# Optimization experiments

Measured on AMD Instinct MI355X. Metric: run time of the kernel, lower is better.

## Reference

```python
import jax, jax.numpy as jnp
import numpy as np

N_NODES = 10000
N_EDGES = 320000
D = 128
H = 4
C = 128
L = 2
NEG_SLOPE = 0.2
LN_EPS = 1e-5


def setup_inputs() -> dict:
    key = jax.random.key(0)
    ks = jax.random.split(key, 8)
    x = jax.random.normal(ks[0], (N_NODES, D), dtype=jnp.float32)
    edge_index = jax.random.randint(ks[1], (2, N_EDGES), 0, N_NODES, dtype=jnp.int64)
    # weights scaled ~Glorot to keep attention logits in a sane range
    Wl = jax.random.normal(ks[2], (L, D, H * C), dtype=jnp.float32) * 0.1
    Wr = jax.random.normal(ks[3], (L, D, H * C), dtype=jnp.float32) * 0.1
    att = jax.random.normal(ks[4], (L, H, C), dtype=jnp.float32) * 0.1
    return {
        "x": x,
        "edge_index": edge_index,
        "Wl": Wl,
        "bl": jnp.zeros((L, H * C), jnp.float32),
        "Wr": Wr,
        "br": jnp.zeros((L, H * C), jnp.float32),
        "att": att,
        "bias": jnp.zeros((L, D), jnp.float32),
        "ln_g": jnp.ones((L, D), jnp.float32),
        "ln_b": jnp.zeros((L, D), jnp.float32),
    }


def _gatv2_layer(x, src, dst, Wl, bl, Wr, br, att, b):
    """GATv2Conv (concat=False -> head mean), messages src->dst, softmax over dst."""
    n = x.shape[0]
    xl = (x @ Wl + bl).reshape(n, H, C)  # source transform
    xr = (x @ Wr + br).reshape(n, H, C)  # target transform
    s = jax.nn.leaky_relu(xl[src] + xr[dst], NEG_SLOPE)  # [E, H, C]
    e = jnp.einsum("ehc,hc->eh", s, att)  # attention logits [E, H]
    m = jax.ops.segment_max(e, dst, num_segments=n)  # stable softmax per dst segment
    ex = jnp.exp(e - m[dst])
    denom = jax.ops.segment_sum(ex, dst, num_segments=n)
    alpha = ex / denom[dst]  # [E, H]
    out = jax.ops.segment_sum(alpha[:, :, None] * xl[src], dst, num_segments=n)  # [N, H, C]
    return out.mean(axis=1) + b  # concat=False -> mean over heads, then bias


def _layer_norm(h, g, b):
    mu = h.mean(-1, keepdims=True)
    var = ((h - mu) ** 2).mean(-1, keepdims=True)
    return (h - mu) * jax.lax.rsqrt(var + LN_EPS) * g + b


def reference(x, edge_index, Wl, bl, Wr, br, att, bias, ln_g, ln_b):
    n = x.shape[0]
    loop = jnp.arange(n, dtype=edge_index.dtype)
    src = jnp.concatenate([edge_index[0], loop])  # add self-loops (PyG default)
    dst = jnp.concatenate([edge_index[1], loop])
    for i in range(L):
        h = _gatv2_layer(x, src, dst, Wl[i], bl[i], Wr[i], br[i], att[i], bias[i])
        x = h + x  # residual
        x = jax.nn.relu(_layer_norm(x, ln_g[i], ln_b[i]))
    return x
```

## Files before the change

### kernel.cpp

```cpp
#include <hip/hip_runtime.h>
#include <math.h>

#define N_NODES 10000
#define N_EDGES 320000
#define E_TOT   (N_EDGES + N_NODES)
#define NEG 0.2f
#define CAP 96

typedef short bf16x8 __attribute__((ext_vector_type(8)));
typedef float f32x4 __attribute__((ext_vector_type(4)));
typedef float f32x2 __attribute__((ext_vector_type(2)));

static __device__ __forceinline__ float4 ld4g(const float* p) { return *(const float4*)p; }

static __device__ __forceinline__ uint4 ldg4(const unsigned short* p, unsigned byteoff) {
    return *(const uint4*)((const char*)p + byteoff);
}
static __device__ __forceinline__ int ldgi(const int* p, int e) { return p[e]; }

static __device__ __forceinline__ unsigned short f2b(float f) {
    unsigned u;
    __builtin_memcpy(&u, &f, 4);
    unsigned r = (u + 0x7fffu + ((u >> 16) & 1u)) >> 16;
    return (unsigned short)r;
}
static __device__ __forceinline__ f32x2 unpk(unsigned d) {
    f32x2 r;
    r.x = __uint_as_float(d << 16);
    r.y = __uint_as_float(d & 0xffff0000u);
    return r;
}

template <int CTRL>
static __device__ __forceinline__ float dpp_add_step(float x) {
    int y = __builtin_amdgcn_update_dpp(0, __float_as_int(x), CTRL, 0xf, 0xf, true);
    return x + __int_as_float(y);
}
static __device__ __forceinline__ float row_sum16(float x) {
    x = dpp_add_step<0x121>(x);
    x = dpp_add_step<0x122>(x);
    x = dpp_add_step<0x124>(x);
    x = dpp_add_step<0x128>(x);
    return x;
}

static __device__ __forceinline__ void comp_full(
    uint4 u,
    const f32x2* __restrict__ xr2, const f32x2* __restrict__ at2,
    f32x2* __restrict__ acc2, float* __restrict__ dsum) {
    const f32x2 neg2 = {NEG, NEG};
    const unsigned* w = (const unsigned*)&u;
    f32x2 F[4];
#pragma unroll
    for (int q = 0; q < 4; ++q) F[q] = unpk(w[q]);
    f32x2 qq = {0.f, 0.f};
#pragma unroll
    for (int q = 0; q < 4; ++q) {
        f32x2 s = F[q] + xr2[q];
        s = __builtin_elementwise_max(s, s * neg2);
        qq = __builtin_elementwise_fma(s, at2[q], qq);
    }
    float ev = __expf(row_sum16(qq.x + qq.y));
    *dsum += ev;
    f32x2 W = {ev, ev};
#pragma unroll
    for (int q = 0; q < 4; ++q)
        acc2[q] = __builtin_elementwise_fma(F[q], W, acc2[q]);
}

static __device__ __forceinline__ void comp_mask(
    uint4 u, bool valid,
    const f32x2* __restrict__ xr2, const f32x2* __restrict__ at2,
    f32x2* __restrict__ acc2, float* __restrict__ dsum) {
    const f32x2 neg2 = {NEG, NEG};
    const unsigned* w = (const unsigned*)&u;
    f32x2 F[4];
#pragma unroll
    for (int q = 0; q < 4; ++q) F[q] = unpk(w[q]);
    f32x2 qq = {0.f, 0.f};
#pragma unroll
    for (int q = 0; q < 4; ++q) {
        f32x2 s = F[q] + xr2[q];
        s = __builtin_elementwise_max(s, s * neg2);
        qq = __builtin_elementwise_fma(s, at2[q], qq);
    }
    float ev = __expf(row_sum16(qq.x + qq.y));
    ev = valid ? ev : 0.f;
    *dsum += ev;
    f32x2 W = {ev, ev};
#pragma unroll
    for (int q = 0; q < 4; ++q)
        acc2[q] = __builtin_elementwise_fma(F[q], W, acc2[q]);
}

__global__ __launch_bounds__(256) void prep_fused_kernel(
    const float* __restrict__ x,
    const float* __restrict__ Wl, const float* __restrict__ Wr,
    unsigned short* __restrict__ xb, unsigned short* __restrict__ WT,
    int* __restrict__ deg) {
    int tid = threadIdx.x, bid = blockIdx.x;
    __shared__ float tbuf[32][33];

    for (int i = bid * 256 + tid; i < N_NODES; i += 256 * 256) deg[i] = 0;

    int l = bid >> 7;
    int rest = bid & 127;
    int ky = rest >> 5, nx = rest & 31;
    int n0 = nx * 32, k0 = ky * 32;
    const float* S = ((n0 < 512) ? Wl : Wr) + (size_t)l * 65536;
    int nn0 = n0 & 511;
    int tx = tid & 31, ty = tid >> 5;
#pragma unroll
    for (int it = 0; it < 4; ++it) {
        int k = k0 + ty + it * 8;
        tbuf[ty + it * 8][tx] = S[(size_t)k * 512 + nn0 + tx];
    }
    __syncthreads();
    unsigned short* dstp = WT + (size_t)l * 1024 * 128;
#pragma unroll
    for (int it = 0; it < 4; ++it) {
        int n = n0 + ty + it * 8;
        int k = k0 + tx;
        dstp[(size_t)n * 128 + k] = f2b(tbuf[tx][ty + it * 8]);
    }
    for (int i = bid * 256 + tid; i < N_NODES * 32; i += 256 * 256) {
        float4 v = ld4g(x + 4 * i);
        ushort4 o = make_ushort4(f2b(v.x), f2b(v.y), f2b(v.z), f2b(v.w));
        *(ushort4*)(xb + 4 * i) = o;
    }
}

template <int DO_FILL>
__global__ __launch_bounds__(256) void gemm_mfma_kernel(const unsigned short* __restrict__ A,
                                                        const unsigned short* __restrict__ Bt,
                                                        const float* __restrict__ bl,
                                                        const float* __restrict__ br,
                                                        unsigned short* __restrict__ xlh,
                                                        unsigned short* __restrict__ xrh,
                                                        const int* __restrict__ ei,
                                                        int* __restrict__ deg,
                                                        int* __restrict__ csr_src) {
    __shared__ unsigned short As[2][64][72];
    int tid = threadIdx.x;
    int wave = tid >> 6, lane = tid & 63;
    int l15 = lane & 15, quad = lane >> 4;
    int row0 = blockIdx.y * 64, col0 = blockIdx.x * 128;
    const float* bias = (col0 < 512) ? (bl + col0) : (br + col0 - 512);

#pragma unroll
    for (int it = 0; it < 4; ++it) {
        int e = tid + it * 256;
        int r = e >> 4, s = e & 15;
        int gr = row0 + r;
        bf16x8 v = (bf16x8)(short)0;
        if (gr < N_NODES) v = *(const bf16x8*)(A + (size_t)gr * 128 + s * 8);
        *(bf16x8*)&As[s >> 3][r][(s & 7) * 8] = v;
    }
    __syncthreads();

    f32x4 acc[8];
#pragma unroll
    for (int ni = 0; ni < 8; ++ni)
#pragma unroll
        for (int r = 0; r < 4; ++r) acc[ni][r] = 0.f;

    const unsigned short* Bbase = Bt + (size_t)col0 * 128;
    unsigned bvo = (unsigned)(l15 * 256 + quad * 16);

#pragma unroll
    for (int kc = 0; kc < 2; ++kc) {
#pragma unroll
        for (int kq = 0; kq < 2; ++kq) {
            bf16x8 af = *(const bf16x8*)&As[kc][wave * 16 + l15][kq * 32 + quad * 8];
            bf16x8 bfr[8];
#pragma unroll
            for (int ni = 0; ni < 8; ++ni) {
                uint4 u = ldg4(Bbase, bvo + (unsigned)(ni * 4096 + kc * 128 + kq * 64));
                __builtin_memcpy(&bfr[ni], &u, 16);
            }
#pragma unroll
            for (int ni = 0; ni < 8; ++ni)
                acc[ni] = __builtin_amdgcn_mfma_f32_16x16x32_bf16(af, bfr[ni], acc[ni], 0, 0, 0);
        }
    }

    float bv[8];
#pragma unroll
    for (int ni = 0; ni < 8; ++ni) bv[ni] = bias[ni * 16 + l15];

    int h = (col0 >> 7) & 3;
    unsigned short* dstb = ((col0 < 512) ? xlh : xrh) + (((size_t)h * N_NODES) << 7);

#pragma unroll
    for (int r = 0; r < 4; ++r) {
        int grow = row0 + wave * 16 + quad * 4 + r;
        if (grow >= N_NODES) continue;
#pragma unroll
        for (int ni = 0; ni < 8; ++ni)
            dstb[((size_t)grow << 7) + ni * 16 + l15] = f2b(acc[ni][r] + bv[ni]);
    }

    if (DO_FILL) {
        bool is64 = ((ei[1] | ei[3] | ei[5] | ei[7]) == 0);
        int nthreads = gridDim.x * gridDim.y * 256;
        int gid = (blockIdx.y * gridDim.x + blockIdx.x) * 256 + tid;
        for (int i = gid; i < E_TOT; i += nthreads) {
            int src, dst;
            if (i < N_EDGES) {
                if (is64) { const long long* e = (const long long*)ei; src = (int)e[i]; dst = (int)e[N_EDGES + i]; }
                else { src = ei[i]; dst = ei[N_EDGES + i]; }
            } else {
                src = dst = i - N_EDGES;
            }
            int pos = atomicAdd(&deg[dst], 1);
            if (pos < CAP) csr_src[dst * CAP + pos] = src;
        }
    }
}

__global__ __launch_bounds__(256) void attn_kernel(
    const unsigned short* __restrict__ xlh,
    const unsigned short* __restrict__ xrh,
    const int* __restrict__ deg, const int* __restrict__ csr_src,
    const float* __restrict__ att,
    float* __restrict__ hpart) {
    int tid = threadIdx.x;
    unsigned bid = blockIdx.x;
    int w = tid >> 6, lane = tid & 63;
    int head = __builtin_amdgcn_readfirstlane((int)((bid & 7u) >> 1));
    int slot = (int)((bid >> 3) * 2 + (bid & 1u));
    int e = lane >> 4, g = lane & 15;
    unsigned gboff = (unsigned)(g << 4);

    const unsigned short* XL = xlh + (((size_t)head * N_NODES) << 7);
    const unsigned short* XR = xrh + (((size_t)head * N_NODES) << 7);
    float* HP = hpart + (((size_t)head * N_NODES) << 7);

    f32x2 at2[4];
    {
        const float* ap = att + head * 128 + g * 8;
        float4 a = ld4g(ap);
        float4 b = ld4g(ap + 4);
        at2[0].x = a.x; at2[0].y = a.y; at2[1].x = a.z; at2[1].y = a.w;
        at2[2].x = b.x; at2[2].y = b.y; at2[3].x = b.z; at2[3].y = b.w;
    }

    for (int dst0 = slot * 4 + w; dst0 < N_NODES; dst0 += 2048) {
        int dst = __builtin_amdgcn_readfirstlane(dst0);

        f32x2 xr2[4];
        {
            uint4 u = *(const uint4*)(XR + ((size_t)dst << 7) + g * 8);
            xr2[0] = unpk(u.x); xr2[1] = unpk(u.y); xr2[2] = unpk(u.z); xr2[3] = unpk(u.w);
        }

        int len = deg[dst];
        if (len > CAP) len = CAP;
        const int* cp = csr_src + dst * CAP;
        int full = len >> 2, rem = len & 3;

        float d = 0.f;
        f32x2 acc2[4] = {{0.f, 0.f}, {0.f, 0.f}, {0.f, 0.f}, {0.f, 0.f}};

        if (full) {
            int idx = ldgi(cp, e);
            uint4 uc = ldg4(XL, ((unsigned)idx << 8) + gboff);
            for (int r = 0; r + 1 < full; ++r) {
                int i1 = ldgi(cp + 4 * (r + 1), e);
                uint4 un = ldg4(XL, ((unsigned)i1 << 8) + gboff);
                comp_full(uc, xr2, at2, acc2, &d);
                uc = un;
            }
            comp_full(uc, xr2, at2, acc2, &d);
        }
        if (rem) {
            int raw = ldgi(cp + 4 * full, e);
            int idx = (e < rem) ? raw : 0;
            uint4 u = ldg4(XL, ((unsigned)idx << 8) + gboff);
            comp_mask(u, e < rem, xr2, at2, acc2, &d);
        }

        float t[8];
#pragma unroll
        for (int q = 0; q < 4; ++q) { t[2 * q] = acc2[q].x; t[2 * q + 1] = acc2[q].y; }
#pragma unroll
        for (int j = 0; j < 8; ++j) {
            t[j] += __shfl_xor(t[j], 16, 64);
            t[j] += __shfl_xor(t[j], 32, 64);
        }
        float ds = d;
        ds += __shfl_xor(ds, 16, 64);
        ds += __shfl_xor(ds, 32, 64);
        float inv = 1.f / ds;
#pragma unroll
        for (int j = 0; j < 8; ++j) t[j] *= inv;

        if (lane < 16) {
            float* op = HP + ((size_t)dst << 7) + g * 8;
            *(float4*)op = make_float4(t[0], t[1], t[2], t[3]);
            *(float4*)(op + 4) = make_float4(t[4], t[5], t[6], t[7]);
        }
    }
}

__global__ __launch_bounds__(256) void combine_kernel(
    const float* __restrict__ hpart, const float* __restrict__ x_in,
    const float* __restrict__ bias, const float* __restrict__ ln_g,
    const float* __restrict__ ln_b, float* __restrict__ x_out,
    unsigned short* __restrict__ xb_out) {
    int wv = (blockIdx.x * blockDim.x + threadIdx.x) >> 6;
    if (wv >= N_NODES) return;
    int lane = threadIdx.x & 63;
    int dst = __builtin_amdgcn_readfirstlane(wv);
    int c = lane * 2;
    const float* hp = hpart + ((size_t)dst << 7) + c;
    const size_t hs = ((size_t)N_NODES) << 7;
    f32x2 h0 = *(const f32x2*)(hp);
    f32x2 h1 = *(const f32x2*)(hp + hs);
    f32x2 h2 = *(const f32x2*)(hp + 2 * hs);
    f32x2 h3 = *(const f32x2*)(hp + 3 * hs);
    f32x2 bi = *(const f32x2*)(bias + c);
    f32x2 xi = *(const f32x2*)(x_in + ((size_t)dst << 7) + c);
    f32x2 hc = ((h0 + h1) + (h2 + h3)) * 0.25f + bi + xi;
    float sm = hc.x + hc.y;
    float sq = hc.x * hc.x + hc.y * hc.y;
    sm = row_sum16(sm); sm += __shfl_xor(sm, 16, 64); sm += __shfl_xor(sm, 32, 64);
    sq = row_sum16(sq); sq += __shfl_xor(sq, 16, 64); sq += __shfl_xor(sq, 32, 64);
    float mu = sm * (1.f / 128.f);
    float var = sq * (1.f / 128.f) - mu * mu;
    float rs = rsqrtf(var + 1e-5f);
    f32x2 gg = *(const f32x2*)(ln_g + c);
    f32x2 bb = *(const f32x2*)(ln_b + c);
    float y0 = fmaxf((hc.x - mu) * rs * gg.x + bb.x, 0.f);
    float y1 = fmaxf((hc.y - mu) * rs * gg.y + bb.y, 0.f);
    f32x2 y = {y0, y1};
    *(f32x2*)(x_out + ((size_t)dst << 7) + c) = y;
    if (xb_out) {
        unsigned pk = ((unsigned)f2b(y0)) | (((unsigned)f2b(y1)) << 16);
        *(unsigned*)(xb_out + ((size_t)dst << 7) + c) = pk;
    }
}

extern "C" void kernel_launch(void* const* d_in, const int* in_sizes, int n_in,
                              void* d_out, int out_size, void* d_ws, size_t ws_size,
                              hipStream_t stream) {
    const float* x    = (const float*)d_in[0];
    const int*   ei   = (const int*)d_in[1];
    const float* Wl   = (const float*)d_in[2];
    const float* bl   = (const float*)d_in[3];
    const float* Wr   = (const float*)d_in[4];
    const float* br   = (const float*)d_in[5];
    const float* att  = (const float*)d_in[6];
    const float* bias = (const float*)d_in[7];
    const float* lng  = (const float*)d_in[8];
    const float* lnb  = (const float*)d_in[9];
    float* out = (float*)d_out;

    char* ws = (char*)d_ws;
    unsigned short* xlh = (unsigned short*)ws; ws += (size_t)4 * N_NODES * 128 * 2;
    unsigned short* xrh = (unsigned short*)ws; ws += (size_t)4 * N_NODES * 128 * 2;
    float* hpart = (float*)ws;          ws += (size_t)4 * N_NODES * 128 * 4;
    float* xbuf  = (float*)ws;          ws += (size_t)N_NODES * 128 * 4;
    unsigned short* xb = (unsigned short*)ws; ws += (size_t)N_NODES * 128 * 2;
    unsigned short* WT = (unsigned short*)ws; ws += (size_t)2 * 1024 * 128 * 2;
    int* deg     = (int*)ws;            ws += (size_t)N_NODES * 4;
    int* csr_src = (int*)ws;            ws += (size_t)N_NODES * CAP * 4;

    prep_fused_kernel<<<256, 256, 0, stream>>>(x, Wl, Wr, xb, WT, deg);

    for (int l = 0; l < 2; ++l) {
        const float* xin = (l == 0) ? x : xbuf;
        float* xout = (l == 0) ? xbuf : out;
        unsigned short* xbo = (l == 0) ? xb : (unsigned short*)nullptr;
        if (l == 0)
            gemm_mfma_kernel<1><<<dim3(8, 157), 256, 0, stream>>>(
                xb, WT, bl, br, xlh, xrh, ei, deg, csr_src);
        else
            gemm_mfma_kernel<0><<<dim3(8, 157), 256, 0, stream>>>(
                xb, WT + (size_t)1024 * 128, bl + 512, br + 512, xlh, xrh, ei, deg, csr_src);
        attn_kernel<<<2048, 256, 0, stream>>>(
            xlh, xrh, deg, csr_src, att + (size_t)l * 512, hpart);
        combine_kernel<<<2500, 256, 0, stream>>>(
            hpart, xin, bias + (size_t)l * 128,
            lng + (size_t)l * 128, lnb + (size_t)l * 128, xout, xbo);
    }
}
```

Before: 239.5 us.

## Stage weight tile in LDS and load A fragments directly in MFMA GEMM

```diff
diff --git a/kernel.cpp b/kernel.cpp
--- a/kernel.cpp
+++ b/kernel.cpp
@@ -140,47 +140,58 @@
                                                         const int* __restrict__ ei,
                                                         int* __restrict__ deg,
                                                         int* __restrict__ csr_src) {
-    __shared__ unsigned short As[2][64][72];
+    __shared__ unsigned short Bs[2][128][72];
     int tid = threadIdx.x;
     int wave = tid >> 6, lane = tid & 63;
     int l15 = lane & 15, quad = lane >> 4;
-    int row0 = blockIdx.y * 64, col0 = blockIdx.x * 128;
+    int row0 = blockIdx.y * 128, col0 = blockIdx.x * 128;
     const float* bias = (col0 < 512) ? (bl + col0) : (br + col0 - 512);
 
-#pragma unroll
-    for (int it = 0; it < 4; ++it) {
-        int e = tid + it * 256;
-        int r = e >> 4, s = e & 15;
-        int gr = row0 + r;
-        bf16x8 v = (bf16x8)(short)0;
-        if (gr < N_NODES) v = *(const bf16x8*)(A + (size_t)gr * 128 + s * 8);
-        *(bf16x8*)&As[s >> 3][r][(s & 7) * 8] = v;
-    }
+    bf16x8 st[8];
+    {
+        const unsigned short* src = Bt + (size_t)(col0 + (tid >> 1)) * 128 + (size_t)(tid & 1) * 64;
+#pragma unroll
+        for (int j = 0; j < 8; ++j) st[j] = *(const bf16x8*)(src + j * 8);
+    }
+
+    bf16x8 af[2][2][2];
+#pragma unroll
+    for (int mi = 0; mi < 2; ++mi) {
+        int row = row0 + wave * 32 + mi * 16 + l15;
+        int rr = (row < N_NODES) ? row : 0;
+        const unsigned short* ap = A + ((size_t)rr << 7);
+#pragma unroll
+        for (int kc = 0; kc < 2; ++kc)
+#pragma unroll
+            for (int kq = 0; kq < 2; ++kq)
+                af[mi][kc][kq] = *(const bf16x8*)(ap + kc * 64 + kq * 32 + quad * 8);
+    }
+
+#pragma unroll
+    for (int j = 0; j < 8; ++j) *(bf16x8*)&Bs[tid & 1][tid >> 1][j * 8] = st[j];
     __syncthreads();
 
-    f32x4 acc[8];
-#pragma unroll
-    for (int ni = 0; ni < 8; ++ni)
-#pragma unroll
-        for (int r = 0; r < 4; ++r) acc[ni][r] = 0.f;
-
-    const unsigned short* Bbase = Bt + (size_t)col0 * 128;
-    unsigned bvo = (unsigned)(l15 * 256 + quad * 16);
+    f32x4 acc[2][8];
+#pragma unroll
+    for (int mi = 0; mi < 2; ++mi)
+#pragma unroll
+        for (int ni = 0; ni < 8; ++ni)
+#pragma unroll
+            for (int r = 0; r < 4; ++r) acc[mi][ni][r] = 0.f;
 
 #pragma unroll
     for (int kc = 0; kc < 2; ++kc) {
 #pragma unroll
         for (int kq = 0; kq < 2; ++kq) {
-            bf16x8 af = *(const bf16x8*)&As[kc][wave * 16 + l15][kq * 32 + quad * 8];
             bf16x8 bfr[8];
 #pragma unroll
-            for (int ni = 0; ni < 8; ++ni) {
-                uint4 u = ldg4(Bbase, bvo + (unsigned)(ni * 4096 + kc * 128 + kq * 64));
-                __builtin_memcpy(&bfr[ni], &u, 16);
-            }
-#pragma unroll
             for (int ni = 0; ni < 8; ++ni)
-                acc[ni] = __builtin_amdgcn_mfma_f32_16x16x32_bf16(af, bfr[ni], acc[ni], 0, 0, 0);
+                bfr[ni] = *(const bf16x8*)&Bs[kc][ni * 16 + l15][kq * 32 + quad * 8];
+#pragma unroll
+            for (int mi = 0; mi < 2; ++mi)
+#pragma unroll
+                for (int ni = 0; ni < 8; ++ni)
+                    acc[mi][ni] = __builtin_amdgcn_mfma_f32_16x16x32_bf16(af[mi][kc][kq], bfr[ni], acc[mi][ni], 0, 0, 0);
         }
     }
 
@@ -192,12 +203,15 @@
     unsigned short* dstb = ((col0 < 512) ? xlh : xrh) + (((size_t)h * N_NODES) << 7);
 
 #pragma unroll
-    for (int r = 0; r < 4; ++r) {
-        int grow = row0 + wave * 16 + quad * 4 + r;
-        if (grow >= N_NODES) continue;
-#pragma unroll
-        for (int ni = 0; ni < 8; ++ni)
-            dstb[((size_t)grow << 7) + ni * 16 + l15] = f2b(acc[ni][r] + bv[ni]);
+    for (int mi = 0; mi < 2; ++mi) {
+#pragma unroll
+        for (int r = 0; r < 4; ++r) {
+            int grow = row0 + wave * 32 + mi * 16 + quad * 4 + r;
+            if (grow >= N_NODES) continue;
+#pragma unroll
+            for (int ni = 0; ni < 8; ++ni)
+                dstb[((size_t)grow << 7) + ni * 16 + l15] = f2b(acc[mi][ni][r] + bv[ni]);
+        }
     }
 
     if (DO_FILL) {
@@ -373,10 +387,10 @@
         float* xout = (l == 0) ? xbuf : out;
         unsigned short* xbo = (l == 0) ? xb : (unsigned short*)nullptr;
         if (l == 0)
-            gemm_mfma_kernel<1><<<dim3(8, 157), 256, 0, stream>>>(
+            gemm_mfma_kernel<1><<<dim3(8, 79), 256, 0, stream>>>(
                 xb, WT, bl, br, xlh, xrh, ei, deg, csr_src);
         else
-            gemm_mfma_kernel<0><<<dim3(8, 157), 256, 0, stream>>>(
+            gemm_mfma_kernel<0><<<dim3(8, 79), 256, 0, stream>>>(
                 xb, WT + (size_t)1024 * 128, bl + 512, br + 512, xlh, xrh, ei, deg, csr_src);
         attn_kernel<<<2048, 256, 0, stream>>>(
             xlh, xrh, deg, csr_src, att + (size_t)l * 512, hpart);
```

After: 210.5 us. 12.1% less time.
